# Optimization experiments

Measured on AMD Instinct MI355X. Metric: run time of the kernel, lower is better.

Reference implementation:

```python
import jax, jax.numpy as jnp
import numpy as np

NUM_HEADS = 16


def setup_inputs() -> dict:
    key = jax.random.key(0)
    ks = jax.random.split(key, 5)
    B, S, E = 4, 2048, 1024
    scale = 1.0 / np.sqrt(E)
    return {
        "x": jax.random.normal(ks[0], (B, S, E), dtype=jnp.float32),
        "w_in": jax.random.normal(ks[1], (E, 3 * E), dtype=jnp.float32) * scale,
        "b_in": jax.random.normal(ks[2], (3 * E,), dtype=jnp.float32) * 0.02,
        "w_out": jax.random.normal(ks[3], (E, E), dtype=jnp.float32) * scale,
        "b_out": jax.random.normal(ks[4], (E,), dtype=jnp.float32) * 0.02,
    }


def reference(x, w_in, b_in, w_out, b_out):
    B, S, E = x.shape
    H = NUM_HEADS
    D = E // H  # head dim
    qkv = x @ w_in + b_in                      # [B,S,3E]
    q, k, v = jnp.split(qkv, 3, axis=-1)       # each [B,S,E]
    q = q.reshape(B, S, H, D)
    k = k.reshape(B, S, H, D)
    v = v.reshape(B, S, H, D)
    # scores scaled by 1/sqrt(D); note: original's causal masked_fill is a
    # no-op (not in-place), so attention is unmasked.
    scores = jnp.einsum("bqhd,bkhd->bhqk", q, k) / jnp.sqrt(jnp.float32(D))
    attn = jax.nn.softmax(scores, axis=-1)      # [B,H,S,S]
    out = jnp.einsum("bhqk,bkhd->bqhd", attn, v).reshape(B, S, E)
    return out @ w_out + b_out
```

## Files before the change

kernel.cpp:

```cpp
#include <hip/hip_runtime.h>
#include <math.h>

#define B_ 4
#define S_ 2048
#define E_ 1024
#define H_ 16
#define D_ 64
#define M_ (B_ * S_)

using f32x4  = __attribute__((ext_vector_type(4))) float;
using short8 = __attribute__((ext_vector_type(8))) short;
using half8  = __attribute__((ext_vector_type(8))) _Float16;
using ushort8_t = __attribute__((ext_vector_type(8))) unsigned short;

__device__ inline unsigned short f2h(float f) {
    _Float16 h = (_Float16)f;
    unsigned short u; __builtin_memcpy(&u, &h, 2); return u;
}
__device__ inline unsigned pk2h(float a, float b) {
    auto t = __builtin_amdgcn_cvt_pkrtz(a, b);
    unsigned u; __builtin_memcpy(&u, &t, 4); return u;
}
__device__ inline float ex2(float x) {
#if __has_builtin(__builtin_amdgcn_exp2f)
    return __builtin_amdgcn_exp2f(x);
#else
    return exp2f(x);
#endif
}
__device__ inline f32x4 mfma16(short8 a, short8 b, f32x4 c) {
    half8 ha, hb;
    __builtin_memcpy(&ha, &a, 16);
    __builtin_memcpy(&hb, &b, 16);
    return __builtin_amdgcn_mfma_f32_16x16x32_f16(ha, hb, c, 0, 0, 0);
}
__device__ inline void gload_lds16(const void* g, void* l) {
    __builtin_amdgcn_global_load_lds(
        (const __attribute__((address_space(1))) void*)g,
        (__attribute__((address_space(3))) void*)l, 16, 0, 0);
}

#define QSCALE 0.18033688f

__global__ __launch_bounds__(256)
void cvt_f16_kernel(const float* __restrict__ X,
                    unsigned short* __restrict__ Xh)
{
    const size_t i = ((size_t)blockIdx.x * 256 + threadIdx.x) * 4;
    float4 v = *(const float4*)(X + i);
    ushort4 h;
    h.x = f2h(v.x);
    h.y = f2h(v.y);
    h.z = f2h(v.z);
    h.w = f2h(v.w);
    *(ushort4*)(Xh + i) = h;
}

__global__ __launch_bounds__(256)
void transpose_cvt_kernel(const float* __restrict__ W,
                          unsigned short* __restrict__ Th, int R, int C)
{
    __shared__ float t[32][33];
    const int tx = threadIdx.x & 31, ty = threadIdx.x >> 5;
    const int c0 = blockIdx.x * 32, r0 = blockIdx.y * 32;
    #pragma unroll
    for (int i = 0; i < 4; ++i)
        t[ty + 8 * i][tx] = W[(size_t)(r0 + ty + 8 * i) * C + c0 + tx];
    __syncthreads();
    #pragma unroll
    for (int i = 0; i < 4; ++i) {
        float v = t[tx][ty + 8 * i];
        Th[(size_t)(c0 + ty + 8 * i) * R + r0 + tx] = f2h(v);
    }
}

template<int OUT_MODE>
__global__ __launch_bounds__(256)
void gemm_mfma_kernel(const unsigned short* __restrict__ Ah,
                      const unsigned short* __restrict__ Bt,
                      const float* __restrict__ bias,
                      float* __restrict__ Cf,
                      unsigned short* __restrict__ Ch,
                      int M, int N, int K)
{
    __shared__ unsigned short As[128][64];
    __shared__ unsigned short Bs[128][64];

    const int tid  = threadIdx.x;
    const int lane = tid & 63;
    const int wave = tid >> 6;
    const int wm = (wave >> 1) * 64, wn = (wave & 1) * 64;
    const int ln = lane & 15, qd = lane >> 4;
    const int m0 = blockIdx.x * 128, n0 = blockIdx.y * 128;

    f32x4 acc[4][4] = {};

    const int srow_l = lane >> 3;
    const int scol   = ((lane & 7) ^ srow_l) * 8;
    const int swz    = (ln & 7) * 8;

    for (int k0 = 0; k0 < K; k0 += 64) {
        #pragma unroll
        for (int c = 0; c < 4; ++c) {
            const int r = wave * 32 + c * 8;
            const size_t ga = (size_t)(m0 + r + srow_l) * K + k0 + scol;
            const size_t gb = (size_t)(n0 + r + srow_l) * K + k0 + scol;
            gload_lds16(Ah + ga, &As[r][0]);
            gload_lds16(Bt + gb, &Bs[r][0]);
        }
        __syncthreads();

        #pragma unroll
        for (int ks = 0; ks < 2; ++ks) {
            const int co = (ks * 32 + qd * 8) ^ swz;
            short8 aa[4], bb[4];
            #pragma unroll
            for (int mt = 0; mt < 4; ++mt)
                aa[mt] = *(const short8*)&As[wm + mt * 16 + ln][co];
            #pragma unroll
            for (int nt = 0; nt < 4; ++nt)
                bb[nt] = *(const short8*)&Bs[wn + nt * 16 + ln][co];
            __builtin_amdgcn_s_setprio(1);
            #pragma unroll
            for (int mt = 0; mt < 4; ++mt)
                #pragma unroll
                for (int nt = 0; nt < 4; ++nt)
                    acc[mt][nt] = mfma16(aa[mt], bb[nt], acc[mt][nt]);
            __builtin_amdgcn_s_setprio(0);
        }
        __syncthreads();
    }

    #pragma unroll
    for (int nt = 0; nt < 4; ++nt) {
        const int col = n0 + wn + nt * 16 + ln;
        const float bv = bias[col];
        const float scale = (OUT_MODE == 2 && col < E_) ? QSCALE : 1.0f;
        #pragma unroll
        for (int mt = 0; mt < 4; ++mt) {
            #pragma unroll
            for (int r = 0; r < 4; ++r) {
                const int row = m0 + wm + mt * 16 + qd * 4 + r;
                float f = acc[mt][nt][r] + bv;
                size_t idx = (size_t)row * N + col;
                if (OUT_MODE == 0) Cf[idx] = f;
                else               Ch[idx] = f2h(f * scale);
            }
        }
    }
}

__global__ __launch_bounds__(256)
void attn_mfma_kernel(const unsigned short* __restrict__ qkvh,
                      unsigned short* __restrict__ outh)
{
    constexpr int TQ = 128, TK = 64, LD = 64;
    __shared__ unsigned short Ksh[TK][LD];
    __shared__ unsigned short Vth[D_][LD];
    __shared__ unsigned short Ps[TQ][LD];

    const int tid  = threadIdx.x;
    const int lane = tid & 63;
    const int wave = tid >> 6;
    const int ln = lane & 15, qd = lane >> 4;
    const int id   = blockIdx.x;
    const int g    = id & 63;
    const int qblk = id >> 6;
    const int h    = g & 15;
    const int b    = g >> 4;
    const int wq0 = wave * 32;
    const int swz = (ln & 7) * 8;

    short8 ones8;
    #pragma unroll
    for (int j = 0; j < 8; ++j) ones8[j] = (short)0x3C00;

    short8 qh[2][2];
    #pragma unroll
    for (int qt = 0; qt < 2; ++qt)
        #pragma unroll
        for (int ks = 0; ks < 2; ++ks) {
            size_t base = ((size_t)(b * S_ + qblk * TQ + wq0 + qt * 16 + ln)) * (3 * E_)
                        + h * 64 + ks * 32 + qd * 8;
            qh[qt][ks] = *(const short8*)(qkvh + base);
        }

    f32x4 o[4][2] = {};
    f32x4 ol[2]   = {};

    const int krow = tid >> 2, kcol = (tid & 3) * 16;
    const int kswz = (krow & 7) * 8;
    const int vkey = (tid & 31) * 2, vdc = (tid >> 5) * 8;

    ushort8_t pk0, pk1, pv0, pv1;
    {
        size_t gb = ((size_t)(b * S_ + krow)) * (3 * E_) + E_ + h * 64 + kcol;
        pk0 = *(const ushort8_t*)(qkvh + gb);
        pk1 = *(const ushort8_t*)(qkvh + gb + 8);
        size_t vb0 = ((size_t)(b * S_ + vkey)) * (3 * E_) + 2 * E_ + h * 64 + vdc;
        pv0 = *(const ushort8_t*)(qkvh + vb0);
        pv1 = *(const ushort8_t*)(qkvh + vb0 + 3 * E_);
    }

    for (int kb = 0; kb < S_; kb += TK) {
        *(ushort8_t*)&Ksh[krow][kcol ^ kswz]       = pk0;
        *(ushort8_t*)&Ksh[krow][(kcol + 8) ^ kswz] = pk1;
        #pragma unroll
        for (int j = 0; j < 8; ++j)
            *(unsigned*)&Vth[vdc + j][vkey ^ (j * 8)] =
                (unsigned)pv0[j] | ((unsigned)pv1[j] << 16);
        __syncthreads();

        if (kb + TK < S_) {
            size_t gb = ((size_t)(b * S_ + kb + TK + krow)) * (3 * E_) + E_ + h * 64 + kcol;
            pk0 = *(const ushort8_t*)(qkvh + gb);
            pk1 = *(const ushort8_t*)(qkvh + gb + 8);
            size_t vb0 = ((size_t)(b * S_ + kb + TK + vkey)) * (3 * E_) + 2 * E_ + h * 64 + vdc;
            pv0 = *(const ushort8_t*)(qkvh + vb0);
            pv1 = *(const ushort8_t*)(qkvh + vb0 + 3 * E_);
        }

        f32x4 st[4][2] = {};
        #pragma unroll
        for (int ks = 0; ks < 2; ++ks) {
            const int co = (ks * 32 + qd * 8) ^ swz;
            short8 kh[4];
            #pragma unroll
            for (int kt = 0; kt < 4; ++kt)
                kh[kt] = *(const short8*)&Ksh[kt * 16 + ln][co];
            __builtin_amdgcn_s_setprio(1);
            #pragma unroll
            for (int kt = 0; kt < 4; ++kt)
                #pragma unroll
                for (int qt = 0; qt < 2; ++qt)
                    st[kt][qt] = mfma16(kh[kt], qh[qt][ks], st[kt][qt]);
            __builtin_amdgcn_s_setprio(0);
        }

        const int pswz = (ln & 7) * 8;
        #pragma unroll
        for (int qt = 0; qt < 2; ++qt)
            #pragma unroll
            for (int kt = 0; kt < 4; ++kt) {
                float p0 = ex2(st[kt][qt][0]);
                float p1 = ex2(st[kt][qt][1]);
                float p2 = ex2(st[kt][qt][2]);
                float p3 = ex2(st[kt][qt][3]);
                uint2 w;
                w.x = pk2h(p0, p1);
                w.y = pk2h(p2, p3);
                *(uint2*)&Ps[wq0 + qt * 16 + ln][(kt * 16 + qd * 4) ^ pswz] = w;
            }

        #pragma unroll
        for (int ks = 0; ks < 2; ++ks) {
            const int co = (ks * 32 + qd * 8) ^ swz;
            short8 vA[4], pB[2];
            #pragma unroll
            for (int dt = 0; dt < 4; ++dt)
                vA[dt] = *(const short8*)&Vth[dt * 16 + ln][co];
            #pragma unroll
            for (int qt = 0; qt < 2; ++qt)
                pB[qt] = *(const short8*)&Ps[wq0 + qt * 16 + ln][co];
            __builtin_amdgcn_s_setprio(1);
            #pragma unroll
            for (int dt = 0; dt < 4; ++dt)
                #pragma unroll
                for (int qt = 0; qt < 2; ++qt)
                    o[dt][qt] = mfma16(vA[dt], pB[qt], o[dt][qt]);
            #pragma unroll
            for (int qt = 0; qt < 2; ++qt)
                ol[qt] = mfma16(ones8, pB[qt], ol[qt]);
            __builtin_amdgcn_s_setprio(0);
        }
        __syncthreads();
    }

    float inv[2];
    #pragma unroll
    for (int qt = 0; qt < 2; ++qt)
        inv[qt] = 1.0f / ol[qt][0];
    #pragma unroll
    for (int qt = 0; qt < 2; ++qt) {
        const int q = qblk * TQ + wq0 + qt * 16 + ln;
        #pragma unroll
        for (int dt = 0; dt < 4; ++dt) {
            size_t base = ((size_t)(b * S_ + q)) * E_ + h * 64 + dt * 16 + qd * 4;
            ushort4 hh;
            #pragma unroll
            for (int r = 0; r < 4; ++r)
                ((unsigned short*)&hh)[r] = f2h(o[dt][qt][r] * inv[qt]);
            *(ushort4*)(outh + base) = hh;
        }
    }
}

extern "C" void kernel_launch(void* const* d_in, const int* in_sizes, int n_in,
                              void* d_out, int out_size, void* d_ws, size_t ws_size,
                              hipStream_t stream)
{
    const float* x     = (const float*)d_in[0];
    const float* w_in  = (const float*)d_in[1];
    const float* b_in  = (const float*)d_in[2];
    const float* w_out = (const float*)d_in[3];
    const float* b_out = (const float*)d_in[4];
    float* outp = (float*)d_out;

    char* ws = (char*)d_ws;
    unsigned short* qkvh  = (unsigned short*)ws;
    unsigned short* attnh = qkvh  + (size_t)M_ * 3 * E_;
    unsigned short* xh    = attnh + (size_t)M_ * E_;
    unsigned short* wInTh  = attnh;
    unsigned short* wOutTh = qkvh;

    cvt_f16_kernel<<<dim3((M_ * E_) / (4 * 256)), 256, 0, stream>>>(x, xh);

    transpose_cvt_kernel<<<dim3(3 * E_ / 32, E_ / 32), 256, 0, stream>>>(
        w_in, wInTh, E_, 3 * E_);

    gemm_mfma_kernel<2><<<dim3(M_ / 128, (3 * E_) / 128), 256, 0, stream>>>(
        xh, wInTh, b_in, nullptr, qkvh, M_, 3 * E_, E_);

    attn_mfma_kernel<<<dim3((S_ / 128) * H_ * B_), 256, 0, stream>>>(
        qkvh, attnh);

    transpose_cvt_kernel<<<dim3(E_ / 32, E_ / 32), 256, 0, stream>>>(
        w_out, wOutTh, E_, E_);

    gemm_mfma_kernel<0><<<dim3(M_ / 128, E_ / 128), 256, 0, stream>>>(
        attnh, wOutTh, b_out, outp, nullptr, M_, E_, E_);
}
```

Baseline: 274.1 us.

## Split attention over key dimension into two partial passes plus combine kernel

```diff
diff --git a/kernel.cpp b/kernel.cpp
--- a/kernel.cpp
+++ b/kernel.cpp
@@ -7,6 +7,8 @@
 #define H_ 16
 #define D_ 64
 #define M_ (B_ * S_)
+#define KSPLIT 2
+#define SPAN (S_ / KSPLIT)
 
 using f32x4  = __attribute__((ext_vector_type(4))) float;
 using short8 = __attribute__((ext_vector_type(8))) short;
@@ -16,6 +18,9 @@
 __device__ inline unsigned short f2h(float f) {
     _Float16 h = (_Float16)f;
     unsigned short u; __builtin_memcpy(&u, &h, 2); return u;
+}
+__device__ inline float h2f(unsigned short u) {
+    _Float16 h; __builtin_memcpy(&h, &u, 2); return (float)h;
 }
 __device__ inline unsigned pk2h(float a, float b) {
     auto t = __builtin_amdgcn_cvt_pkrtz(a, b);
@@ -152,7 +157,8 @@
 
 __global__ __launch_bounds__(256)
 void attn_mfma_kernel(const unsigned short* __restrict__ qkvh,
-                      unsigned short* __restrict__ outh)
+                      unsigned short* __restrict__ oS,
+                      float* __restrict__ lS)
 {
     constexpr int TQ = 128, TK = 64, LD = 64;
     __shared__ unsigned short Ksh[TK][LD];
@@ -163,13 +169,15 @@
     const int lane = tid & 63;
     const int wave = tid >> 6;
     const int ln = lane & 15, qd = lane >> 4;
-    const int id   = blockIdx.x;
-    const int g    = id & 63;
-    const int qblk = id >> 6;
-    const int h    = g & 15;
-    const int b    = g >> 4;
+    const int id    = blockIdx.x;
+    const int g     = id & 63;
+    const int qblk  = (id >> 6) & 15;
+    const int split = id >> 10;
+    const int h     = g & 15;
+    const int b     = g >> 4;
     const int wq0 = wave * 32;
     const int swz = (ln & 7) * 8;
+    const int kb0 = split * SPAN;
 
     short8 ones8;
     #pragma unroll
@@ -194,15 +202,15 @@
 
     ushort8_t pk0, pk1, pv0, pv1;
     {
-        size_t gb = ((size_t)(b * S_ + krow)) * (3 * E_) + E_ + h * 64 + kcol;
+        size_t gb = ((size_t)(b * S_ + kb0 + krow)) * (3 * E_) + E_ + h * 64 + kcol;
         pk0 = *(const ushort8_t*)(qkvh + gb);
         pk1 = *(const ushort8_t*)(qkvh + gb + 8);
-        size_t vb0 = ((size_t)(b * S_ + vkey)) * (3 * E_) + 2 * E_ + h * 64 + vdc;
+        size_t vb0 = ((size_t)(b * S_ + kb0 + vkey)) * (3 * E_) + 2 * E_ + h * 64 + vdc;
         pv0 = *(const ushort8_t*)(qkvh + vb0);
         pv1 = *(const ushort8_t*)(qkvh + vb0 + 3 * E_);
     }
 
-    for (int kb = 0; kb < S_; kb += TK) {
+    for (int kb = kb0; kb < kb0 + SPAN; kb += TK) {
         *(ushort8_t*)&Ksh[krow][kcol ^ kswz]       = pk0;
         *(ushort8_t*)&Ksh[krow][(kcol + 8) ^ kswz] = pk1;
         #pragma unroll
@@ -211,7 +219,7 @@
                 (unsigned)pv0[j] | ((unsigned)pv1[j] << 16);
         __syncthreads();
 
-        if (kb + TK < S_) {
+        if (kb + TK < kb0 + SPAN) {
             size_t gb = ((size_t)(b * S_ + kb + TK + krow)) * (3 * E_) + E_ + h * 64 + kcol;
             pk0 = *(const ushort8_t*)(qkvh + gb);
             pk1 = *(const ushort8_t*)(qkvh + gb + 8);
@@ -276,23 +284,42 @@
         __syncthreads();
     }
 
-    float inv[2];
-    #pragma unroll
-    for (int qt = 0; qt < 2; ++qt)
-        inv[qt] = 1.0f / ol[qt][0];
     #pragma unroll
     for (int qt = 0; qt < 2; ++qt) {
         const int q = qblk * TQ + wq0 + qt * 16 + ln;
+        const size_t row = (size_t)b * S_ + q;
+        if (qd == 0)
+            lS[(size_t)split * M_ * H_ + row * H_ + h] = ol[qt][0];
         #pragma unroll
         for (int dt = 0; dt < 4; ++dt) {
-            size_t base = ((size_t)(b * S_ + q)) * E_ + h * 64 + dt * 16 + qd * 4;
+            size_t base = (size_t)split * M_ * E_ + row * E_ + h * 64 + dt * 16 + qd * 4;
             ushort4 hh;
             #pragma unroll
             for (int r = 0; r < 4; ++r)
-                ((unsigned short*)&hh)[r] = f2h(o[dt][qt][r] * inv[qt]);
-            *(ushort4*)(outh + base) = hh;
-        }
-    }
+                ((unsigned short*)&hh)[r] = f2h(o[dt][qt][r]);
+            *(ushort4*)(oS + base) = hh;
+        }
+    }
+}
+
+__global__ __launch_bounds__(256)
+void combine_kernel(const unsigned short* __restrict__ oS,
+                    const float* __restrict__ lS,
+                    unsigned short* __restrict__ outh)
+{
+    const size_t i = ((size_t)blockIdx.x * 256 + threadIdx.x) * 8;
+    const size_t row = i >> 10;
+    const int h = (int)((i & 1023) >> 6);
+    ushort8_t a = *(const ushort8_t*)(oS + i);
+    ushort8_t c = *(const ushort8_t*)(oS + (size_t)M_ * E_ + i);
+    const float la = lS[row * H_ + h];
+    const float lb = lS[(size_t)M_ * H_ + row * H_ + h];
+    const float inv = 1.0f / (la + lb);
+    ushort8_t r;
+    #pragma unroll
+    for (int j = 0; j < 8; ++j)
+        r[j] = f2h((h2f(a[j]) + h2f(c[j])) * inv);
+    *(ushort8_t*)(outh + i) = r;
 }
 
 extern "C" void kernel_launch(void* const* d_in, const int* in_sizes, int n_in,
@@ -310,6 +337,8 @@
     unsigned short* qkvh  = (unsigned short*)ws;
     unsigned short* attnh = qkvh  + (size_t)M_ * 3 * E_;
     unsigned short* xh    = attnh + (size_t)M_ * E_;
+    unsigned short* oS    = xh    + (size_t)M_ * E_;
+    float*          lS    = (float*)(oS + (size_t)KSPLIT * M_ * E_);
     unsigned short* wInTh  = attnh;
     unsigned short* wOutTh = qkvh;
 
@@ -321,8 +350,10 @@
     gemm_mfma_kernel<2><<<dim3(M_ / 128, (3 * E_) / 128), 256, 0, stream>>>(
         xh, wInTh, b_in, nullptr, qkvh, M_, 3 * E_, E_);
 
-    attn_mfma_kernel<<<dim3((S_ / 128) * H_ * B_), 256, 0, stream>>>(
-        qkvh, attnh);
+    attn_mfma_kernel<<<dim3((S_ / 128) * H_ * B_ * KSPLIT), 256, 0, stream>>>(
+        qkvh, oS, lS);
+
+    combine_kernel<<<dim3((M_ * E_) / (8 * 256)), 256, 0, stream>>>(oS, lS, attnh);
 
     transpose_cvt_kernel<<<dim3(E_ / 32, E_ / 32), 256, 0, stream>>>(
         w_out, wOutTh, E_, E_);
```

Result: slower. 302.3 us (+10.3%).

## Keep softmax probabilities in registers and software-pipeline PV with next QK tile

Applied to the files above, without the earlier changes.

```diff
diff --git a/kernel.cpp b/kernel.cpp
--- a/kernel.cpp
+++ b/kernel.cpp
@@ -156,8 +156,8 @@
 {
     constexpr int TQ = 128, TK = 64, LD = 64;
     __shared__ unsigned short Ksh[TK][LD];
-    __shared__ unsigned short Vth[D_][LD];
-    __shared__ unsigned short Ps[TQ][LD];
+    __shared__ unsigned short VthA[D_][LD];
+    __shared__ unsigned short VthB[D_][LD];
 
     const int tid  = threadIdx.x;
     const int lane = tid & 63;
@@ -187,10 +187,19 @@
 
     f32x4 o[4][2] = {};
     f32x4 ol[2]   = {};
+    short8 pBp[2][2] = {};
 
     const int krow = tid >> 2, kcol = (tid & 3) * 16;
     const int kswz = (krow & 7) * 8;
     const int vkey = (tid & 31) * 2, vdc = (tid >> 5) * 8;
+    const int vslot = (vkey & 0x23) | ((vkey & 0x0C) << 1) | ((vkey & 0x10) >> 2);
+
+    {
+        ushort8_t z = {};
+        unsigned short* p = &VthB[0][0];
+        *(ushort8_t*)(p + tid * 8)        = z;
+        *(ushort8_t*)(p + 2048 + tid * 8) = z;
+    }
 
     ushort8_t pk0, pk1, pv0, pv1;
     {
@@ -202,78 +211,98 @@
         pv1 = *(const ushort8_t*)(qkvh + vb0 + 3 * E_);
     }
 
-    for (int kb = 0; kb < S_; kb += TK) {
-        *(ushort8_t*)&Ksh[krow][kcol ^ kswz]       = pk0;
-        *(ushort8_t*)&Ksh[krow][(kcol + 8) ^ kswz] = pk1;
-        #pragma unroll
-        for (int j = 0; j < 8; ++j)
-            *(unsigned*)&Vth[vdc + j][vkey ^ (j * 8)] =
-                (unsigned)pv0[j] | ((unsigned)pv1[j] << 16);
-        __syncthreads();
-
-        if (kb + TK < S_) {
-            size_t gb = ((size_t)(b * S_ + kb + TK + krow)) * (3 * E_) + E_ + h * 64 + kcol;
-            pk0 = *(const ushort8_t*)(qkvh + gb);
-            pk1 = *(const ushort8_t*)(qkvh + gb + 8);
-            size_t vb0 = ((size_t)(b * S_ + kb + TK + vkey)) * (3 * E_) + 2 * E_ + h * 64 + vdc;
-            pv0 = *(const ushort8_t*)(qkvh + vb0);
-            pv1 = *(const ushort8_t*)(qkvh + vb0 + 3 * E_);
-        }
-
-        f32x4 st[4][2] = {};
-        #pragma unroll
-        for (int ks = 0; ks < 2; ++ks) {
-            const int co = (ks * 32 + qd * 8) ^ swz;
-            short8 kh[4];
-            #pragma unroll
-            for (int kt = 0; kt < 4; ++kt)
-                kh[kt] = *(const short8*)&Ksh[kt * 16 + ln][co];
-            __builtin_amdgcn_s_setprio(1);
-            #pragma unroll
-            for (int kt = 0; kt < 4; ++kt)
-                #pragma unroll
-                for (int qt = 0; qt < 2; ++qt)
-                    st[kt][qt] = mfma16(kh[kt], qh[qt][ks], st[kt][qt]);
-            __builtin_amdgcn_s_setprio(0);
-        }
-
-        const int pswz = (ln & 7) * 8;
+    #define TILE_BODY(VW, VR, PREFETCH_KB, DO_PREFETCH)                        \
+    {                                                                          \
+        *(ushort8_t*)&Ksh[krow][kcol ^ kswz]       = pk0;                      \
+        *(ushort8_t*)&Ksh[krow][(kcol + 8) ^ kswz] = pk1;                      \
+        _Pragma("unroll")                                                      \
+        for (int j = 0; j < 8; ++j)                                            \
+            *(unsigned*)&VW[vdc + j][vslot ^ (j * 8)] =                        \
+                (unsigned)pv0[j] | ((unsigned)pv1[j] << 16);                   \
+        __syncthreads();                                                       \
+        if (DO_PREFETCH) {                                                     \
+            size_t gb_ = ((size_t)(b * S_ + (PREFETCH_KB) + krow)) * (3 * E_)  \
+                       + E_ + h * 64 + kcol;                                   \
+            pk0 = *(const ushort8_t*)(qkvh + gb_);                             \
+            pk1 = *(const ushort8_t*)(qkvh + gb_ + 8);                         \
+            size_t vb_ = ((size_t)(b * S_ + (PREFETCH_KB) + vkey)) * (3 * E_)  \
+                       + 2 * E_ + h * 64 + vdc;                                \
+            pv0 = *(const ushort8_t*)(qkvh + vb_);                             \
+            pv1 = *(const ushort8_t*)(qkvh + vb_ + 3 * E_);                    \
+        }                                                                      \
+        f32x4 st[4][2] = {};                                                   \
+        _Pragma("unroll")                                                      \
+        for (int ks = 0; ks < 2; ++ks) {                                       \
+            const int co = (ks * 32 + qd * 8) ^ swz;                           \
+            short8 kh[4];                                                      \
+            _Pragma("unroll")                                                  \
+            for (int kt = 0; kt < 4; ++kt)                                     \
+                kh[kt] = *(const short8*)&Ksh[kt * 16 + ln][co];               \
+            __builtin_amdgcn_s_setprio(1);                                     \
+            _Pragma("unroll")                                                  \
+            for (int kt = 0; kt < 4; ++kt)                                     \
+                _Pragma("unroll")                                              \
+                for (int qt = 0; qt < 2; ++qt)                                 \
+                    st[kt][qt] = mfma16(kh[kt], qh[qt][ks], st[kt][qt]);       \
+            __builtin_amdgcn_s_setprio(0);                                     \
+        }                                                                      \
+                \
+        _Pragma("unroll")                                                      \
+        for (int ks = 0; ks < 2; ++ks) {                                       \
+            const int co = (ks * 32 + qd * 8) ^ swz;                           \
+            short8 vA[4];                                                      \
+            _Pragma("unroll")                                                  \
+            for (int dt = 0; dt < 4; ++dt)                                     \
+                vA[dt] = *(const short8*)&VR[dt * 16 + ln][co];                \
+            __builtin_amdgcn_s_setprio(1);                                     \
+            _Pragma("unroll")                                                  \
+            for (int dt = 0; dt < 4; ++dt)                                     \
+                _Pragma("unroll")                                              \
+                for (int qt = 0; qt < 2; ++qt)                                 \
+                    o[dt][qt] = mfma16(vA[dt], pBp[ks][qt], o[dt][qt]);        \
+            _Pragma("unroll")                                                  \
+            for (int qt = 0; qt < 2; ++qt)                                     \
+                ol[qt] = mfma16(ones8, pBp[ks][qt], ol[qt]);                   \
+            __builtin_amdgcn_s_setprio(0);                                     \
+        }                                                                      \
+                             \
+        _Pragma("unroll")                                                      \
+        for (int qt = 0; qt < 2; ++qt)                                         \
+            _Pragma("unroll")                                                  \
+            for (int ks = 0; ks < 2; ++ks) {                                   \
+                unsigned w_[4];                                                \
+                w_[0] = pk2h(ex2(st[2 * ks][qt][0]), ex2(st[2 * ks][qt][1]));  \
+                w_[1] = pk2h(ex2(st[2 * ks][qt][2]), ex2(st[2 * ks][qt][3]));  \
+                w_[2] = pk2h(ex2(st[2 * ks + 1][qt][0]),                       \
+                             ex2(st[2 * ks + 1][qt][1]));                      \
+                w_[3] = pk2h(ex2(st[2 * ks + 1][qt][2]),                       \
+                             ex2(st[2 * ks + 1][qt][3]));                      \
+                __builtin_memcpy(&pBp[ks][qt], w_, 16);                        \
+            }                                                                  \
+        __syncthreads();                                                       \
+    }
+
+    for (int kb = 0; kb < S_; kb += 2 * TK) {
+        TILE_BODY(VthA, VthB, kb + TK, true);
+        TILE_BODY(VthB, VthA, kb + 2 * TK, (kb + 2 * TK < S_));
+    }
+    #undef TILE_BODY
+
+    #pragma unroll
+    for (int ks = 0; ks < 2; ++ks) {
+        const int co = (ks * 32 + qd * 8) ^ swz;
+        short8 vA[4];
+        #pragma unroll
+        for (int dt = 0; dt < 4; ++dt)
+            vA[dt] = *(const short8*)&VthB[dt * 16 + ln][co];
+        #pragma unroll
+        for (int dt = 0; dt < 4; ++dt)
+            #pragma unroll
+            for (int qt = 0; qt < 2; ++qt)
+                o[dt][qt] = mfma16(vA[dt], pBp[ks][qt], o[dt][qt]);
         #pragma unroll
         for (int qt = 0; qt < 2; ++qt)
-            #pragma unroll
-            for (int kt = 0; kt < 4; ++kt) {
-                float p0 = ex2(st[kt][qt][0]);
-                float p1 = ex2(st[kt][qt][1]);
-                float p2 = ex2(st[kt][qt][2]);
-                float p3 = ex2(st[kt][qt][3]);
-                uint2 w;
-                w.x = pk2h(p0, p1);
-                w.y = pk2h(p2, p3);
-                *(uint2*)&Ps[wq0 + qt * 16 + ln][(kt * 16 + qd * 4) ^ pswz] = w;
-            }
-
-        #pragma unroll
-        for (int ks = 0; ks < 2; ++ks) {
-            const int co = (ks * 32 + qd * 8) ^ swz;
-            short8 vA[4], pB[2];
-            #pragma unroll
-            for (int dt = 0; dt < 4; ++dt)
-                vA[dt] = *(const short8*)&Vth[dt * 16 + ln][co];
-            #pragma unroll
-            for (int qt = 0; qt < 2; ++qt)
-                pB[qt] = *(const short8*)&Ps[wq0 + qt * 16 + ln][co];
-            __builtin_amdgcn_s_setprio(1);
-            #pragma unroll
-            for (int dt = 0; dt < 4; ++dt)
-                #pragma unroll
-                for (int qt = 0; qt < 2; ++qt)
-                    o[dt][qt] = mfma16(vA[dt], pB[qt], o[dt][qt]);
-            #pragma unroll
-            for (int qt = 0; qt < 2; ++qt)
-                ol[qt] = mfma16(ones8, pB[qt], ol[qt]);
-            __builtin_amdgcn_s_setprio(0);
-        }
-        __syncthreads();
+            ol[qt] = mfma16(ones8, pBp[ks][qt], ol[qt]);
     }
 
     float inv[2];
```

New measurement: 278.7 us. About the same (+1.7%).
